# Performance work log

Hardware: AMD Instinct MI355X
Metric: run time of the kernel (lower is better)

## Reference

```python
import jax, jax.numpy as jnp
import numpy as np

C = 192          # filter_channels (= in_channels in this module)
K = 3            # kernel_size
NB = 10          # num_bins of rational-quadratic spline (VITS default)
TB = 5.0         # tail_bound
NF = 4           # number of ConvFlow steps per branch
L = 3            # DDSConv n_layers
LOG2PI = float(np.log(2.0 * np.pi))


def conv1x1(x, w, b):
    # x: (B, Cin, T), w: (Cout, Cin)
    return jnp.einsum('oi,bit->bot', w, x) + b[None, :, None]


def depthwise(x, w, b, dil):
    # x: (B, C, T), w: (C, 1, K), dilated depthwise conv, 'same' padding
    pad = dil * (K - 1) // 2
    y = jax.lax.conv_general_dilated(
        x, w, window_strides=(1,), padding=[(pad, pad)], rhs_dilation=(dil,),
        dimension_numbers=('NCH', 'OIH', 'NCH'), feature_group_count=x.shape[1])
    return y + b[None, :, None]


def layer_norm_c(x, g, b, eps=1e-5):
    # VITS LayerNorm: normalize over the channel axis (axis=1)
    m = jnp.mean(x, axis=1, keepdims=True)
    v = jnp.mean((x - m) ** 2, axis=1, keepdims=True)
    return (x - m) * jax.lax.rsqrt(v + eps) * g[None, :, None] + b[None, :, None]


def dds(x, x_mask, g, dep_w, dep_b, pw_w, pw_b, ln_g, ln_b):
    # DDSConv: dilated depth-separable conv stack with residual
    if g is not None:
        x = x + g
    for i in range(L):
        dil = K ** i
        y = depthwise(x * x_mask, dep_w[i], dep_b[i], dil)
        y = jax.nn.gelu(layer_norm_c(y, ln_g[i, 0], ln_b[i, 0]))
        y = conv1x1(y, pw_w[i], pw_b[i])
        y = jax.nn.gelu(layer_norm_c(y, ln_g[i, 1], ln_b[i, 1]))
        x = x + y  # dropout disabled in deterministic reference
    return x * x_mask


def ew_affine(z, x_mask, m, logs):
    y = (m[None, :, None] + jnp.exp(logs)[None, :, None] * z) * x_mask
    ld = jnp.sum(logs[None, :, None] * x_mask, axis=(1, 2))
    return y, ld


def rqs_forward(x_in, uw, uh, ud):
    # unconstrained rational-quadratic spline, forward direction, linear tails
    mb = 1e-3  # min bin width / height / derivative
    const = float(np.log(np.expm1(1.0 - mb)))
    inside = (x_in >= -TB) & (x_in <= TB)
    ud = jnp.pad(ud, ((0, 0), (0, 0), (0, 0), (1, 1)), constant_values=const)
    wd = jax.nn.softmax(uw, -1); wd = mb + (1.0 - mb * NB) * wd
    cw = jnp.cumsum(wd, -1)
    cw = jnp.concatenate([jnp.zeros_like(cw[..., :1]), cw], -1)
    cw = 2.0 * TB * cw - TB
    cw = cw.at[..., 0].set(-TB).at[..., -1].set(TB)
    wd = cw[..., 1:] - cw[..., :-1]
    ht = jax.nn.softmax(uh, -1); ht = mb + (1.0 - mb * NB) * ht
    ch = jnp.cumsum(ht, -1)
    ch = jnp.concatenate([jnp.zeros_like(ch[..., :1]), ch], -1)
    ch = 2.0 * TB * ch - TB
    ch = ch.at[..., 0].set(-TB).at[..., -1].set(TB)
    ht = ch[..., 1:] - ch[..., :-1]
    dv = mb + jax.nn.softplus(ud)  # (..., NB+1)
    xc = jnp.clip(x_in, -TB, TB)
    idx = jnp.clip(jnp.sum((xc[..., None] >= cw[..., :-1]).astype(jnp.int32), -1) - 1, 0, NB - 1)
    g = lambda a, i: jnp.take_along_axis(a, i[..., None], -1)[..., 0]
    icw, iw, ich, ih = g(cw, idx), g(wd, idx), g(ch, idx), g(ht, idx)
    idelta = ih / iw
    d0, d1 = g(dv, idx), g(dv, idx + 1)
    th = (xc - icw) / iw
    t1m = th * (1.0 - th)
    den = idelta + (d0 + d1 - 2.0 * idelta) * t1m
    out = ich + ih * (idelta * th * th + d0 * t1m) / den
    dnum = idelta * idelta * (d1 * th * th + 2.0 * idelta * t1m + d0 * (1.0 - th) ** 2)
    lad = jnp.log(dnum) - 2.0 * jnp.log(den)
    return jnp.where(inside, out, x_in), jnp.where(inside, lad, 0.0)


def conv_flow(z, x_mask, g, pre_w, pre_b, dep_w, dep_b, pw_w, pw_b, ln_g, ln_b, proj_w, proj_b):
    x0, x1 = z[:, :1], z[:, 1:]  # (B,1,T) each
    h = conv1x1(x0, pre_w, pre_b)
    h = dds(h, x_mask, g, dep_w, dep_b, pw_w, pw_b, ln_g, ln_b)
    h = conv1x1(h, proj_w, proj_b) * x_mask      # (B, 3*NB-1, T)
    B, _, T = h.shape
    h = h.reshape(B, 1, 3 * NB - 1, T).transpose(0, 1, 3, 2)  # (B,1,T,3*NB-1)
    s = 1.0 / np.sqrt(C)
    x1n, lad = rqs_forward(x1, h[..., :NB] * s, h[..., NB:2 * NB] * s, h[..., 2 * NB:])
    zo = jnp.concatenate([x0, x1n], 1) * x_mask
    return zo, jnp.sum(lad * x_mask, axis=(1, 2))


def _forward(x, x_mask, w, e_q, pre_w, pre_b, proj_w, proj_b,
             dds_dep_w, dds_dep_b, dds_pw_w, dds_pw_b, dds_ln_g, dds_ln_b,
             post_pre_w, post_pre_b, post_proj_w, post_proj_b,
             pdds_dep_w, pdds_dep_b, pdds_pw_w, pdds_pw_b, pdds_ln_g, pdds_ln_b,
             aff_m, aff_logs,
             f_pre_w, f_pre_b, f_dep_w, f_dep_b, f_pw_w, f_pw_b, f_ln_g, f_ln_b, f_proj_w, f_proj_b,
             paff_m, paff_logs,
             p_pre_w, p_pre_b, p_dep_w, p_dep_b, p_pw_w, p_pw_b, p_ln_g, p_ln_b, p_proj_w, p_proj_b):
    x = jax.lax.stop_gradient(x)
    h = conv1x1(x, pre_w, pre_b)
    h = dds(h, x_mask, None, dds_dep_w, dds_dep_b, dds_pw_w, dds_pw_b, dds_ln_g, dds_ln_b)
    h = conv1x1(h, proj_w, proj_b) * x_mask
    hw = conv1x1(w, post_pre_w, post_pre_b)
    hw = dds(hw, x_mask, None, pdds_dep_w, pdds_dep_b, pdds_pw_w, pdds_pw_b, pdds_ln_g, pdds_ln_b)
    hw = conv1x1(hw, post_proj_w, post_proj_b) * x_mask
    e = e_q * x_mask
    zq, ldq = ew_affine(e, x_mask, paff_m, paff_logs)
    gp = h + hw
    for i in range(NF):
        zq, ld = conv_flow(zq, x_mask, gp, p_pre_w[i], p_pre_b[i], p_dep_w[i], p_dep_b[i],
                           p_pw_w[i], p_pw_b[i], p_ln_g[i], p_ln_b[i], p_proj_w[i], p_proj_b[i])
        ldq = ldq + ld
        zq = zq[:, ::-1]  # Flip (logdet 0)
    zu, z1 = zq[:, :1], zq[:, 1:]
    u = jax.nn.sigmoid(zu) * x_mask
    z0 = (w - u) * x_mask
    ldq = ldq + jnp.sum((jax.nn.log_sigmoid(zu) + jax.nn.log_sigmoid(-zu)) * x_mask, axis=(1, 2))
    logq = jnp.sum(-0.5 * (LOG2PI + e * e) * x_mask, axis=(1, 2)) - ldq
    y0 = jnp.log(jnp.maximum(z0, 1e-5)) * x_mask  # Log flow
    ldt = jnp.sum(-y0, axis=(1, 2))
    z = jnp.concatenate([y0, z1], 1)
    z, ld = ew_affine(z, x_mask, aff_m, aff_logs)
    ldt = ldt + ld
    for i in range(NF):
        z, ld = conv_flow(z, x_mask, h, f_pre_w[i], f_pre_b[i], f_dep_w[i], f_dep_b[i],
                          f_pw_w[i], f_pw_b[i], f_ln_g[i], f_ln_b[i], f_proj_w[i], f_proj_b[i])
        ldt = ldt + ld
        z = z[:, ::-1]
    nll = jnp.sum(0.5 * (LOG2PI + z * z) * x_mask, axis=(1, 2)) - ldt
    return nll + logq  # (B,)


def setup_inputs() -> dict:
    key = jax.random.key(0)
    ks = jax.random.split(key, 24)
    B, T = 32, 768
    P = 3 * NB - 1
    r = lambda k, shape, s=0.05: jax.random.normal(k, shape, jnp.float32) * s
    d = {}
    d['x'] = jax.random.normal(ks[0], (B, C, T), jnp.float32)
    d['x_mask'] = jnp.ones((B, 1, T), jnp.float32)
    d['w'] = jax.random.uniform(ks[1], (B, 1, T), jnp.float32) * 10.0 + 1.0  # positive durations
    d['e_q'] = jax.random.normal(ks[2], (B, 2, T), jnp.float32)
    d['pre_w'] = r(ks[3], (C, C)); d['pre_b'] = jnp.zeros((C,), jnp.float32)
    d['proj_w'] = r(ks[4], (C, C)); d['proj_b'] = jnp.zeros((C,), jnp.float32)
    d['dds_dep_w'] = r(ks[5], (L, C, 1, K)); d['dds_dep_b'] = jnp.zeros((L, C), jnp.float32)
    d['dds_pw_w'] = r(ks[6], (L, C, C)); d['dds_pw_b'] = jnp.zeros((L, C), jnp.float32)
    d['dds_ln_g'] = jnp.ones((L, 2, C), jnp.float32); d['dds_ln_b'] = jnp.zeros((L, 2, C), jnp.float32)
    d['post_pre_w'] = r(ks[7], (C, 1)); d['post_pre_b'] = jnp.zeros((C,), jnp.float32)
    d['post_proj_w'] = r(ks[8], (C, C)); d['post_proj_b'] = jnp.zeros((C,), jnp.float32)
    d['pdds_dep_w'] = r(ks[9], (L, C, 1, K)); d['pdds_dep_b'] = jnp.zeros((L, C), jnp.float32)
    d['pdds_pw_w'] = r(ks[10], (L, C, C)); d['pdds_pw_b'] = jnp.zeros((L, C), jnp.float32)
    d['pdds_ln_g'] = jnp.ones((L, 2, C), jnp.float32); d['pdds_ln_b'] = jnp.zeros((L, 2, C), jnp.float32)
    d['aff_m'] = r(ks[11], (2,)); d['aff_logs'] = r(ks[12], (2,))
    d['f_pre_w'] = r(ks[13], (NF, C, 1)); d['f_pre_b'] = jnp.zeros((NF, C), jnp.float32)
    d['f_dep_w'] = r(ks[14], (NF, L, C, 1, K)); d['f_dep_b'] = jnp.zeros((NF, L, C), jnp.float32)
    d['f_pw_w'] = r(ks[15], (NF, L, C, C)); d['f_pw_b'] = jnp.zeros((NF, L, C), jnp.float32)
    d['f_ln_g'] = jnp.ones((NF, L, 2, C), jnp.float32); d['f_ln_b'] = jnp.zeros((NF, L, 2, C), jnp.float32)
    d['f_proj_w'] = r(ks[16], (NF, P, C), 0.01); d['f_proj_b'] = jnp.zeros((NF, P), jnp.float32)
    d['paff_m'] = r(ks[17], (2,)); d['paff_logs'] = r(ks[18], (2,))
    d['p_pre_w'] = r(ks[19], (NF, C, 1)); d['p_pre_b'] = jnp.zeros((NF, C), jnp.float32)
    d['p_dep_w'] = r(ks[20], (NF, L, C, 1, K)); d['p_dep_b'] = jnp.zeros((NF, L, C), jnp.float32)
    d['p_pw_w'] = r(ks[21], (NF, L, C, C)); d['p_pw_b'] = jnp.zeros((NF, L, C), jnp.float32)
    d['p_ln_g'] = jnp.ones((NF, L, 2, C), jnp.float32); d['p_ln_b'] = jnp.zeros((NF, L, 2, C), jnp.float32)
    d['p_proj_w'] = r(ks[22], (NF, P, C), 0.01); d['p_proj_b'] = jnp.zeros((NF, P), jnp.float32)
    return d


def reference(x, x_mask, w, e_q, pre_w, pre_b, proj_w, proj_b,
              dds_dep_w, dds_dep_b, dds_pw_w, dds_pw_b, dds_ln_g, dds_ln_b,
              post_pre_w, post_pre_b, post_proj_w, post_proj_b,
              pdds_dep_w, pdds_dep_b, pdds_pw_w, pdds_pw_b, pdds_ln_g, pdds_ln_b,
              aff_m, aff_logs,
              f_pre_w, f_pre_b, f_dep_w, f_dep_b, f_pw_w, f_pw_b, f_ln_g, f_ln_b, f_proj_w, f_proj_b,
              paff_m, paff_logs,
              p_pre_w, p_pre_b, p_dep_w, p_dep_b, p_pw_w, p_pw_b, p_ln_g, p_ln_b, p_proj_w, p_proj_b):
    return _forward(x, x_mask, w, e_q, pre_w, pre_b, proj_w, proj_b,
                    dds_dep_w, dds_dep_b, dds_pw_w, dds_pw_b, dds_ln_g, dds_ln_b,
                    post_pre_w, post_pre_b, post_proj_w, post_proj_b,
                    pdds_dep_w, pdds_dep_b, pdds_pw_w, pdds_pw_b, pdds_ln_g, pdds_ln_b,
                    aff_m, aff_logs,
                    f_pre_w, f_pre_b, f_dep_w, f_dep_b, f_pw_w, f_pw_b, f_ln_g, f_ln_b, f_proj_w, f_proj_b,
                    paff_m, paff_logs,
                    p_pre_w, p_pre_b, p_dep_w, p_dep_b, p_pw_w, p_pw_b, p_ln_g, p_ln_b, p_proj_w, p_proj_b)
```

## Files before the change

kernel.cpp:

```cpp
#include <hip/hip_runtime.h>
#include <math.h>

#define CC 192
#define TTT 768
#define PP 29
#define LOG2PI_F 1.8378770664093453f
#define WSLOT 36864
#define PSW 6144
#define XS 200
#define XSP 200
#define PARL 1728

typedef __attribute__((ext_vector_type(8))) short short8;
typedef __attribute__((ext_vector_type(4))) float floatx4;
typedef __attribute__((ext_vector_type(2))) float float2v;
union Frag { int4 i; short8 s; };

__device__ __forceinline__ float2v fma2(float2v a, float2v b, float2v c){
  return __builtin_elementwise_fma(a, b, c);
}
__device__ __forceinline__ float geluf(float x){
  float u = 1.5957691216057308f * (x + 0.044715f*x*x*x);
  return x * __builtin_amdgcn_rcpf(1.f + __expf(-u));
}
__device__ __forceinline__ float softplus_f(float x){
  return (x > 20.f) ? x : log1pf(__expf(x));
}
__device__ __forceinline__ float logsig_f(float x){
  return -softplus_f(-x);
}
__device__ __forceinline__ unsigned short f2bf(float f){
  unsigned int u = __builtin_bit_cast(unsigned int, f);
  u += 0x7fffu + ((u >> 16) & 1u);
  return (unsigned short)(u >> 16);
}
__device__ __forceinline__ unsigned int packbf2(float a0, float a1){
  return (unsigned int)f2bf(a0) | ((unsigned int)f2bf(a1) << 16);
}
__device__ __forceinline__ void unbf2(unsigned int u, float& lo, float& hi){
  lo = __builtin_bit_cast(float, u << 16);
  hi = __builtin_bit_cast(float, u & 0xffff0000u);
}
__device__ __forceinline__ float2v unbf2v(unsigned int u){
  float2v r;
  r.x = __builtin_bit_cast(float, u << 16);
  r.y = __builtin_bit_cast(float, u & 0xffff0000u);
  return r;
}
__device__ __forceinline__ void unp8(int4 v, float* o){
  unsigned int* p = (unsigned int*)&v;
  unbf2(p[0], o[0], o[1]); unbf2(p[1], o[2], o[3]);
  unbf2(p[2], o[4], o[5]); unbf2(p[3], o[6], o[7]);
}
__device__ __forceinline__ void f4arr(float4 v, float* o){ o[0]=v.x;o[1]=v.y;o[2]=v.z;o[3]=v.w; }
__device__ __forceinline__ float2v pick2(float4 a, float4 b, int p){
  switch(p){
    case 0: return (float2v){a.x, a.y};
    case 1: return (float2v){a.z, a.w};
    case 2: return (float2v){b.x, b.y};
    default: return (float2v){b.z, b.w};
  }
}

__global__ __launch_bounds__(256) void convert_w_k(
    const float* __restrict__ p0, const float* __restrict__ p1,
    const float* __restrict__ p2, const float* __restrict__ p3,
    const float* __restrict__ p4, const float* __restrict__ p5,
    const float* __restrict__ p6, const float* __restrict__ p7,
    const float* __restrict__ p8, unsigned short* __restrict__ Wb){
  int i = blockIdx.x*256 + threadIdx.x;
  const int totalA = 33*WSLOT;
  const int total = totalA + 8*PSW;
  if (i >= total) return;
  if (i < totalA){
    int slot = i / WSLOT, j = i % WSLOT;
    int e = j & 7, lane = (j>>3) & 63, kt = j >> 9;
    int k = kt % 6, tile = kt / 6;
    int co = tile*16 + (lane & 15);
    int kk = k*32 + (lane>>4)*8 + e;
    int r = co*CC + kk;
    const float* src;
    if      (slot == 0) src = p0 + r;
    else if (slot == 1) src = p1 + r;
    else if (slot == 2) src = p2 + r;
    else if (slot < 6)  src = p3 + (size_t)(slot-3)*WSLOT + r;
    else if (slot < 9)  src = p4 + (size_t)(slot-6)*WSLOT + r;
    else if (slot < 21) src = p5 + (size_t)(slot-9)*WSLOT + r;
    else                src = p6 + (size_t)(slot-21)*WSLOT + r;
    Wb[i] = f2bf(*src);
  } else {
    int r2 = i - totalA;
    int ps = r2 / PSW, j = r2 % PSW;
    int e = j & 7, lane = (j>>3) & 63, kt = j >> 9;
    int k = kt % 6, tile = kt / 6;
    int co = tile*16 + (lane & 15); if (co > PP-1) co = PP-1;
    int kk = k*32 + (lane>>4)*8 + e;
    const float* base = (ps < 4) ? (p7 + (size_t)ps*PP*CC) : (p8 + (size_t)(ps-4)*PP*CC);
    Wb[i] = f2bf(base[co*CC + kk]);
  }
}

__global__ __launch_bounds__(256) void pack_par_k(
    const float* __restrict__ dds_dep_w, const float* __restrict__ dds_dep_b,
    const float* __restrict__ dds_ln_g,  const float* __restrict__ dds_ln_b,
    const float* __restrict__ dds_pw_b,
    const float* __restrict__ pdds_dep_w, const float* __restrict__ pdds_dep_b,
    const float* __restrict__ pdds_ln_g,  const float* __restrict__ pdds_ln_b,
    const float* __restrict__ pdds_pw_b,
    const float* __restrict__ p_dep_w, const float* __restrict__ p_dep_b,
    const float* __restrict__ p_ln_g,  const float* __restrict__ p_ln_b,
    const float* __restrict__ p_pw_b,
    const float* __restrict__ f_dep_w, const float* __restrict__ f_dep_b,
    const float* __restrict__ f_ln_g,  const float* __restrict__ f_ln_b,
    const float* __restrict__ f_pw_b,
    float* __restrict__ P){
  int i = blockIdx.x*256 + threadIdx.x;
  const int total = 30*PARL;
  if (i >= total) return;
  int ls = i / PARL, r = i % PARL;
  int arr = r / 192, c = r % 192;
  const float *dep_w, *dep_b, *ln_g, *ln_b, *pw_b;
  int l;
  if (ls < 3){
    l = ls; dep_w = dds_dep_w; dep_b = dds_dep_b; ln_g = dds_ln_g; ln_b = dds_ln_b; pw_b = dds_pw_b;
  } else if (ls < 6){
    l = ls-3; dep_w = pdds_dep_w; dep_b = pdds_dep_b; ln_g = pdds_ln_g; ln_b = pdds_ln_b; pw_b = pdds_pw_b;
  } else if (ls < 18){
    int f = (ls-6)/3; l = (ls-6)%3;
    dep_w = p_dep_w + (size_t)f*3*CC*3; dep_b = p_dep_b + (size_t)f*3*CC;
    ln_g = p_ln_g + (size_t)f*3*2*CC;  ln_b = p_ln_b + (size_t)f*3*2*CC;
    pw_b = p_pw_b + (size_t)f*3*CC;
  } else {
    int f = (ls-18)/3; l = (ls-18)%3;
    dep_w = f_dep_w + (size_t)f*3*CC*3; dep_b = f_dep_b + (size_t)f*3*CC;
    ln_g = f_ln_g + (size_t)f*3*2*CC;  ln_b = f_ln_b + (size_t)f*3*2*CC;
    pw_b = f_pw_b + (size_t)f*3*CC;
  }
  float v;
  if      (arr < 3)  v = dep_w[((size_t)l*CC + c)*3 + arr];
  else if (arr == 3) v = dep_b[(size_t)l*CC + c];
  else if (arr == 4) v = ln_g[((size_t)l*2+0)*CC + c];
  else if (arr == 5) v = ln_b[((size_t)l*2+0)*CC + c];
  else if (arr == 6) v = ln_g[((size_t)l*2+1)*CC + c];
  else if (arr == 7) v = ln_b[((size_t)l*2+1)*CC + c];
  else               v = pw_b[(size_t)l*CC + c];
  P[i] = v;
}

__global__ __launch_bounds__(256) void transpose_x_k(
    const float* __restrict__ x, unsigned short* __restrict__ xT){
  __shared__ unsigned short tile[32*XS];
  int b = blockIdx.y, t0 = blockIdx.x*32, tid = threadIdx.x;
  int tl4 = (tid & 7)*4, cr = tid >> 3;
  #pragma unroll
  for (int rnd=0; rnd<6; rnd++){
    int c = rnd*32 + cr;
    float4 v4 = *(const float4*)(x + ((size_t)b*CC + c)*TTT + t0 + tl4);
    tile[(tl4+0)*XS + c] = f2bf(v4.x);
    tile[(tl4+1)*XS + c] = f2bf(v4.y);
    tile[(tl4+2)*XS + c] = f2bf(v4.z);
    tile[(tl4+3)*XS + c] = f2bf(v4.w);
  }
  __syncthreads();
  #pragma unroll
  for (int k=0;k<3;k++){
    int task = k*256 + tid;
    int row = task/24, cn = task%24;
    *(int4*)(xT + ((size_t)b*TTT + t0 + row)*CC + cn*8) = *(const int4*)&tile[row*XS + cn*8];
  }
}

__global__ __launch_bounds__(256) void conv_cc_k(
    const unsigned short* __restrict__ in, const unsigned short* __restrict__ Wsw,
    const float* __restrict__ bias, const float* __restrict__ mask,
    const unsigned short* __restrict__ addsrc, unsigned short* __restrict__ outb, int mode){
  __shared__ unsigned short bufX[32*XS];
  __shared__ unsigned short bufY[32*XS];
  __shared__ float marr[32];
  int b = blockIdx.y, t0 = blockIdx.x*32, tid = threadIdx.x;
  #pragma unroll
  for (int k=0;k<3;k++){
    int task = k*256 + tid;
    int row = task/24, cn = task%24;
    const unsigned short* src = in + ((size_t)b*TTT + t0 + row)*CC + cn*8;
    *(int4*)&bufX[row*XS + cn*8] = *(const int4*)src;
    if (mode == 2){
      const unsigned short* s2 = addsrc + ((size_t)b*TTT + t0 + row)*CC + cn*8;
      *(int4*)&bufY[row*XS + cn*8] = *(const int4*)s2;
    }
  }
  if (tid >= 128 && tid < 160) marr[tid-128] = mask[(size_t)b*TTT + t0 + (tid-128)];
  __syncthreads();
  int w = tid >> 6, lane = tid & 63;
  int n16 = lane & 15, quad = lane >> 4;
  Frag af[3][6];
  #pragma unroll
  for (int ct=0; ct<3; ct++){
    int tile = w*3 + ct;
    #pragma unroll
    for (int k=0;k<6;k++)
      af[ct][k].i = *(const int4*)(Wsw + ((size_t)(tile*6 + k)*64 + lane)*8);
  }
  floatx4 acc[3][2];
  #pragma unroll
  for (int ct=0;ct<3;ct++)
    #pragma unroll
    for (int tt=0;tt<2;tt++)
      acc[ct][tt] = (floatx4){0.f,0.f,0.f,0.f};
  #pragma unroll
  for (int k=0;k<6;k++){
    Frag bf[2];
    #pragma unroll
    for (int tt=0;tt<2;tt++)
      bf[tt].i = *(const int4*)&bufX[(tt*16+n16)*XS + k*32 + quad*8];
    #pragma unroll
    for (int ct=0;ct<3;ct++)
      #pragma unroll
      for (int tt=0;tt<2;tt++)
        acc[ct][tt] = __builtin_amdgcn_mfma_f32_16x16x32_bf16(af[ct][k].s, bf[tt].s, acc[ct][tt], 0,0,0);
  }
  __syncthreads();
  #pragma unroll
  for (int ct=0;ct<3;ct++){
    int cobase = w*48 + ct*16 + quad*4;
    float4 b4 = *(const float4*)(bias + cobase);
    float ba[4] = {b4.x, b4.y, b4.z, b4.w};
    #pragma unroll
    for (int tt=0;tt<2;tt++){
      int t = tt*16 + n16;
      float mv = (mode >= 1) ? marr[t] : 1.f;
      float av[4] = {0.f,0.f,0.f,0.f};
      if (mode == 2){
        uint2 uy = *(uint2*)&bufY[t*XS + cobase];
        unbf2(uy.x, av[0], av[1]); unbf2(uy.y, av[2], av[3]);
      }
      float hh[4];
      #pragma unroll
      for (int r=0;r<4;r++){
        float v = acc[ct][tt][r] + ba[r];
        if (mode >= 1) v *= mv;
        if (mode == 2) v += av[r];
        hh[r] = v;
      }
      uint2 wv; wv.x = packbf2(hh[0], hh[1]); wv.y = packbf2(hh[2], hh[3]);
      *(uint2*)&bufX[t*XS + cobase] = wv;
    }
  }
  __syncthreads();
  #pragma unroll
  for (int k=0;k<3;k++){
    int task = k*256 + tid;
    int row = task/24, cn = task%24;
    *(int4*)(outb + ((size_t)b*TTT + t0 + row)*CC + cn*8) = *(const int4*)&bufX[row*XS + cn*8];
  }
}

template<int DIL, int SPLITF>
__device__ __forceinline__ void dds_layer(
    unsigned short* __restrict__ ping,
    const float* __restrict__ pl,
    float* __restrict__ pnd, const float* __restrict__ pns,
    const float* __restrict__ mrow,
    float (* __restrict__ sqx)[2][2],
    const unsigned short* __restrict__ WL,
    int tid, int w, int lane, int n16, int quad, int row){
  constexpr int NT = SPLITF ? 6 : 12;
  const int tb = SPLITF ? ((w & 1)*6) : 0;
  const int rowL = SPLITF ? (16 + (w>>1)*16 + n16) : row;
  Frag bfr[6];
  floatx4 acc[NT];
  {
    int iL = rowL - DIL; iL = iL < 0 ? 0 : iL;
    int iR = rowL + DIL; iR = iR > 63 ? 63 : iR;
    float2v vv[24];
    float2v s2v = {0.f,0.f}, q2v = {0.f,0.f};
    #pragma unroll
    for (int j=0;j<6;j++){
      int kk = j*32 + quad*8;
      int4 L4 = *(const int4*)&ping[iL*XSP + kk];
      int4 C4 = *(const int4*)&ping[rowL*XSP + kk];
      int4 R4 = *(const int4*)&ping[iR*XSP + kk];
      unsigned int* Lp = (unsigned int*)&L4;
      unsigned int* Cp = (unsigned int*)&C4;
      unsigned int* Rp = (unsigned int*)&R4;
      float4 w0a = *(const float4*)&pl[kk],       w0b = *(const float4*)&pl[kk+4];
      float4 w1a = *(const float4*)&pl[192+kk],   w1b = *(const float4*)&pl[192+kk+4];
      float4 w2a = *(const float4*)&pl[384+kk],   w2b = *(const float4*)&pl[384+kk+4];
      float4 dba = *(const float4*)&pl[576+kk],   dbb = *(const float4*)&pl[576+kk+4];
      #pragma unroll
      for (int p=0;p<4;p++){
        float2v val = fma2(pick2(w0a,w0b,p), unbf2v(Lp[p]),
                      fma2(pick2(w1a,w1b,p), unbf2v(Cp[p]),
                      fma2(pick2(w2a,w2b,p), unbf2v(Rp[p]), pick2(dba,dbb,p))));
        vv[j*4+p] = val;
        s2v += val;
        q2v = fma2(val, val, q2v);
      }
    }
    float s = s2v.x + s2v.y, q = q2v.x + q2v.y;
    s += __shfl_xor(s, 16); s += __shfl_xor(s, 32);
    q += __shfl_xor(q, 16); q += __shfl_xor(q, 32);
    float mm = s*(1.f/CC);
    float rr = rsqrtf(q*(1.f/CC) - mm*mm + 1e-5f);
    float2v mm2 = {mm,mm}, rr2 = {rr,rr};
    #pragma unroll
    for (int j=0;j<6;j++){
      int kk = j*32 + quad*8;
      float4 g0a = *(const float4*)&pl[768+kk], g0b = *(const float4*)&pl[768+kk+4];
      float4 b0a = *(const float4*)&pl[960+kk], b0b = *(const float4*)&pl[960+kk+4];
      unsigned int wwp[4];
      #pragma unroll
      for (int p=0;p<4;p++){
        float2v a = fma2((vv[j*4+p]-mm2)*rr2, pick2(g0a,g0b,p), pick2(b0a,b0b,p));
        wwp[p] = packbf2(geluf(a.x), geluf(a.y));
      }
      bfr[j].i = make_int4((int)wwp[0], (int)wwp[1], (int)wwp[2], (int)wwp[3]);
    }
  }
  __syncthreads();
  if (pns){
    #pragma unroll
    for (int k=0;k<7;k++){
      int i2 = k*256 + tid;
      if (i2 < PARL) pnd[i2] = pns[i2];
    }
  }
  {
    Frag afb[2][6];
    #pragma unroll
    for (int k=0;k<6;k++)
      afb[0][k].i = *(const int4*)(WL + ((size_t)((tb+0)*6 + k)*64 + lane)*8);
    #pragma unroll
    for (int tile=0; tile<NT; tile++){
      int cur = tile & 1, nxt = cur ^ 1;
      if (tile < NT-1){
        #pragma unroll
        for (int k=0;k<6;k++)
          afb[nxt][k].i = *(const int4*)(WL + ((size_t)((tb+tile+1)*6 + k)*64 + lane)*8);
      }
      acc[tile] = (floatx4){0.f,0.f,0.f,0.f};
      #pragma unroll
      for (int k=0;k<6;k++)
        acc[tile] = __builtin_amdgcn_mfma_f32_16x16x32_bf16(afb[cur][k].s, bfr[k].s, acc[tile], 0,0,0);
    }
  }
  float2v s2p = {0.f,0.f}, q2p = {0.f,0.f};
  #pragma unroll
  for (int tile=0; tile<NT; tile++){
    int co = (tb+tile)*16 + quad*4;
    float4 pbv = *(const float4*)&pl[1536+co];
    acc[tile][0] += pbv.x; acc[tile][1] += pbv.y;
    acc[tile][2] += pbv.z; acc[tile][3] += pbv.w;
    float2v v01 = {acc[tile][0], acc[tile][1]};
    float2v v23 = {acc[tile][2], acc[tile][3]};
    s2p += v01 + v23;
    q2p = fma2(v01, v01, q2p);
    q2p = fma2(v23, v23, q2p);
  }
  float s2 = s2p.x + s2p.y, q2 = q2p.x + q2p.y;
  s2 += __shfl_xor(s2, 16); s2 += __shfl_xor(s2, 32);
  q2 += __shfl_xor(q2, 16); q2 += __shfl_xor(q2, 32);
  if constexpr (SPLITF){
    int r16 = rowL - 16;
    if (quad == 0){ sqx[r16][w&1][0] = s2; sqx[r16][w&1][1] = q2; }
    __syncthreads();
    int oh = (w&1)^1;
    s2 += sqx[r16][oh][0];
    q2 += sqx[r16][oh][1];
  }
  float cmP = s2*(1.f/CC);
  float crP = rsqrtf(q2*(1.f/CC) - cmP*cmP + 1e-5f);
  float mc = mrow[rowL];
  float2v mc2 = {mc,mc};
  float2v cm2 = {cmP,cmP}, cr2 = {crP,crP};
  #pragma unroll
  for (int tile=0; tile<NT; tile++){
    int co = (tb+tile)*16 + quad*4;
    float4 g1v = *(const float4*)&pl[1152+co];
    float4 b1v = *(const float4*)&pl[1344+co];
    uint2 ux = *(uint2*)&ping[rowL*XSP + co];
    float2v x01 = unbf2v(ux.x), x23 = unbf2v(ux.y);
    float2v v01 = {acc[tile][0], acc[tile][1]};
    float2v v23 = {acc[tile][2], acc[tile][3]};
    float2v a01 = fma2((v01-cm2)*cr2, (float2v){g1v.x,g1v.y}, (float2v){b1v.x,b1v.y});
    float2v a23 = fma2((v23-cm2)*cr2, (float2v){g1v.z,g1v.w}, (float2v){b1v.z,b1v.w});
    float2v h01 = (x01 + (float2v){geluf(a01.x), geluf(a01.y)}) * mc2;
    float2v h23 = (x23 + (float2v){geluf(a23.x), geluf(a23.y)}) * mc2;
    uint2 wv;
    wv.x = packbf2(h01.x, h01.y);
    wv.y = packbf2(h23.x, h23.y);
    *(uint2*)&ping[rowL*XSP + co] = wv;
  }
  __syncthreads();
}

__global__ __launch_bounds__(256,3) void mega_dds_k(
    const unsigned short* __restrict__ in,
    const float* __restrict__ zsrc, int zstride,
    const unsigned short* __restrict__ g,
    unsigned short* __restrict__ outb,
    const float* __restrict__ mask,
    const float* __restrict__ parP,
    const float* __restrict__ pw1, const float* __restrict__ pb1,
    const unsigned short* __restrict__ Wsw,
    int srcmode, int outmode,
    const unsigned short* __restrict__ projW, const float* __restrict__ projB,
    float* __restrict__ z, int zs, float* __restrict__ acco){
  __shared__ unsigned short ping[64*XSP];
  __shared__ float par[2][PARL];
  __shared__ float mrow[64];
  __shared__ float sqx[32][2][2];
  float* pro = par[0];

  int b = blockIdx.y, t0 = blockIdx.x*32, tid = threadIdx.x;
  int ws0 = t0 - 16;
  int w = tid >> 6, lane = tid & 63;
  int n16 = lane & 15, quad = lane >> 4;
  int row = w*16 + n16;
  const float* mkb = mask + (size_t)b*TTT;

  if (tid < 64){
    int gt = ws0 + tid;
    bool inr = (gt >= 0) && (gt < TTT);
    int gc = gt < 0 ? 0 : (gt > TTT-1 ? TTT-1 : gt);
    mrow[tid] = inr ? mkb[gc] : 0.f;
  }
  #pragma unroll
  for (int k=0;k<7;k++){
    int i2 = k*256 + tid;
    if (i2 < PARL) par[0][i2] = parP[i2];
  }
  if (srcmode == 0){
    #pragma unroll
    for (int k=0;k<6;k++){
      int task = k*256 + tid;
      int r = task/24, cn = task%24, c0 = cn*8;
      int gt = ws0 + r;
      bool inr = (gt >= 0) && (gt < TTT);
      int gc = gt < 0 ? 0 : (gt > TTT-1 ? TTT-1 : gt);
      float mv = inr ? mkb[gc] : 0.f;
      float hv[8];
      unp8(*(const int4*)(in + ((size_t)b*TTT + gc)*CC + c0), hv);
      int4 pk;
      pk.x = (int)packbf2(hv[0]*mv, hv[1]*mv); pk.y = (int)packbf2(hv[2]*mv, hv[3]*mv);
      pk.z = (int)packbf2(hv[4]*mv, hv[5]*mv); pk.w = (int)packbf2(hv[6]*mv, hv[7]*mv);
      *(int4*)&ping[r*XSP + c0] = pk;
    }
  } else {
    #pragma unroll
    for (int k=0;k<6;k++){
      int task = k*256 + tid;
      int r = task/24, cn = task%24, c0 = cn*8;
      int gt = ws0 + r;
      bool inr = (gt >= 0) && (gt < TTT);
      int gc = gt < 0 ? 0 : (gt > TTT-1 ? TTT-1 : gt);
      float mv = inr ? mkb[gc] : 0.f;
      float zv = inr ? zsrc[(size_t)b*zstride + gc] : 0.f;
      float hv[8];
      if (g){
        unp8(*(const int4*)(g + ((size_t)b*TTT + gc)*CC + c0), hv);
      } else {
        #pragma unroll
        for (int e=0;e<8;e++) hv[e] = 0.f;
      }
      float4 pwa = *(const float4*)(pw1 + c0);
      float4 pwb2 = *(const float4*)(pw1 + c0 + 4);
      float4 pba = *(const float4*)(pb1 + c0);
      float4 pbb2 = *(const float4*)(pb1 + c0 + 4);
      float pwv[8], pbv[8];
      f4arr(pwa, pwv); f4arr(pwb2, pwv+4);
      f4arr(pba, pbv); f4arr(pbb2, pbv+4);
      float ov[8];
      #pragma unroll
      for (int e=0;e<8;e++) ov[e] = (hv[e] + fmaf(pwv[e], zv, pbv[e]))*mv;
      int4 pk;
      pk.x = (int)packbf2(ov[0], ov[1]); pk.y = (int)packbf2(ov[2], ov[3]);
      pk.z = (int)packbf2(ov[4], ov[5]); pk.w = (int)packbf2(ov[6], ov[7]);
      *(int4*)&ping[r*XSP + c0] = pk;
    }
  }
  __syncthreads();

  dds_layer<1,0>(ping, par[0], par[1], parP + (size_t)1*PARL, mrow, sqx,
                 Wsw + 0*(size_t)WSLOT, tid, w, lane, n16, quad, row);
  dds_layer<3,0>(ping, par[1], par[0], parP + (size_t)2*PARL, mrow, sqx,
                 Wsw + 1*(size_t)WSLOT, tid, w, lane, n16, quad, row);
  dds_layer<9,1>(ping, par[0], nullptr, nullptr, mrow, sqx,
                 Wsw + 2*(size_t)WSLOT, tid, w, lane, n16, quad, row);

  if (outmode == 0){
    #pragma unroll
    for (int k=0;k<3;k++){
      int task = k*256 + tid;
      int r = task/24, cn = task%24, c0 = cn*8;
      *(int4*)(outb + ((size_t)b*TTT + t0 + r)*CC + c0) = *(const int4*)&ping[(16+r)*XSP + c0];
    }
    return;
  }

  {
    int ctp = w & 1;
    int prow = 16 + (w>>1)*16 + n16;
    Frag afp[6];
    #pragma unroll
    for (int k=0;k<6;k++)
      afp[k].i = *(const int4*)(projW + ((size_t)(ctp*6 + k)*64 + lane)*8);
    Frag bfp[6];
    #pragma unroll
    for (int k=0;k<6;k++)
      bfp[k].i = *(const int4*)&ping[prow*XSP + k*32 + quad*8];
    floatx4 acc2 = (floatx4){0.f,0.f,0.f,0.f};
    #pragma unroll
    for (int k=0;k<6;k++)
      acc2 = __builtin_amdgcn_mfma_f32_16x16x32_bf16(afp[k].s, bfp[k].s, acc2, 0,0,0);
    int rt = prow - 16;
    float mv = mrow[prow];
    #pragma unroll
    for (int r=0;r<4;r++){
      int co = ctp*16 + quad*4 + r;
      if (co < PP) pro[rt*30 + co] = (acc2[r] + projB[co]) * mv;
    }
  }
  __syncthreads();
  if (tid < 32){
    const float scv = 0.07216878364870323f;
    int tg = t0 + tid;
    float m = mrow[16+tid];
    float* z0p = z + ((size_t)b*2 + zs)*TTT + tg;
    float* z1p = z + ((size_t)b*2 + (1-zs))*TTT + tg;
    float xs = *z1p;
    float uw[10], uh[10], ud[9];
    #pragma unroll
    for (int k=0;k<10;k++) uw[k]=pro[tid*30+k]*scv;
    #pragma unroll
    for (int k=0;k<10;k++) uh[k]=pro[tid*30+10+k]*scv;
    #pragma unroll
    for (int k=0;k<9;k++)  ud[k]=pro[tid*30+20+k];
    bool inside = (xs >= -5.f) && (xs <= 5.f);
    float xc = fminf(fmaxf(xs,-5.f),5.f);
    float mx=uw[0];
    #pragma unroll
    for (int k=1;k<10;k++) mx=fmaxf(mx,uw[k]);
    float sw=0.f; float wd[10];
    #pragma unroll
    for (int k=0;k<10;k++){ wd[k]=__expf(uw[k]-mx); sw+=wd[k]; }
    float invw = 1.f/sw;
    #pragma unroll
    for (int k=0;k<10;k++) wd[k]=fmaf(0.99f*invw, wd[k], 1e-3f);
    float mh=uh[0];
    #pragma unroll
    for (int k=1;k<10;k++) mh=fmaxf(mh,uh[k]);
    float sh=0.f; float ht[10];
    #pragma unroll
    for (int k=0;k<10;k++){ ht[k]=__expf(uh[k]-mh); sh+=ht[k]; }
    float invh = 1.f/sh;
    #pragma unroll
    for (int k=0;k<10;k++) ht[k]=fmaf(0.99f*invh, ht[k], 1e-3f);
    float cw=-5.f, icw=-5.f, iw=1.f; int idx=0;
    #pragma unroll
    for (int i2=0;i2<10;i2++){
      float nw = (i2==9) ? 5.f : fmaf(10.f, wd[i2], cw);
      if (cw <= xc){ idx=i2; icw=cw; iw=nw-cw; }
      cw=nw;
    }
    float ch=-5.f, ich=-5.f, ih=1.f;
    #pragma unroll
    for (int i2=0;i2<10;i2++){
      float nh = (i2==9) ? 5.f : fmaf(10.f, ht[i2], ch);
      if (i2==idx){ ich=ch; ih=nh-ch; }
      ch=nh;
    }
    const float UDC = logf(expm1f(0.999f));
    float d0=1.f, d1=1.f;
    #pragma unroll
    for (int k=0;k<11;k++){
      float uu = (k==0 || k==10) ? UDC : ud[k-1];
      float dk = 1e-3f + softplus_f(uu);
      if (k==idx)   d0=dk;
      if (k==idx+1) d1=dk;
    }
    float idel = ih/iw;
    float th = (xc-icw)/iw;
    float t1m = th*(1.f-th);
    float den = idel + (d0+d1-2.f*idel)*t1m;
    float outv = ich + ih*(idel*th*th + d0*t1m)/den;
    float omt = 1.f-th;
    float dnum = idel*idel*(d1*th*th + 2.f*idel*t1m + d0*omt*omt);
    float lad = logf(dnum) - 2.f*logf(den);
    float y = inside ? outv : xs;
    lad = inside ? lad : 0.f;
    *z1p = y*m;
    *z0p = (*z0p)*m;
    float lm = lad*m;
    lm += __shfl_xor(lm, 1); lm += __shfl_xor(lm, 2);
    lm += __shfl_xor(lm, 4); lm += __shfl_xor(lm, 8);
    lm += __shfl_xor(lm, 16);
    if (tid == 0) atomicAdd(acco + b, -lm);
  }
}

__global__ __launch_bounds__(256) void init_z_k(
    const float* __restrict__ e_q, const float* __restrict__ mask,
    const float* __restrict__ pm, const float* __restrict__ pl,
    float* __restrict__ z, float* __restrict__ acc){
  __shared__ float red[256];
  int b = blockIdx.y; int t = blockIdx.x*256 + threadIdx.x;
  float m = mask[(size_t)b*TTT + t];
  float pl0=pl[0], pl1=pl[1];
  float e0 = e_q[((size_t)b*2+0)*TTT + t]*m;
  float e1 = e_q[((size_t)b*2+1)*TTT + t]*m;
  z[((size_t)b*2+0)*TTT + t] = fmaf(__expf(pl0), e0, pm[0])*m;
  z[((size_t)b*2+1)*TTT + t] = fmaf(__expf(pl1), e1, pm[1])*m;
  float contrib = -0.5f*(LOG2PI_F + e0*e0)*m - 0.5f*(LOG2PI_F + e1*e1)*m - (pl0+pl1)*m;
  int tid = threadIdx.x;
  red[tid] = contrib;
  __syncthreads();
  for (int o=128;o>0;o>>=1){ if (tid<o) red[tid]+=red[tid+o]; __syncthreads(); }
  if (tid==0) atomicAdd(acc+b, red[0]);
}

__global__ __launch_bounds__(256) void final_pre_k(
    float* __restrict__ z, const float* __restrict__ w_in, const float* __restrict__ mask,
    const float* __restrict__ am, const float* __restrict__ al, float* __restrict__ acc){
  __shared__ float red[256];
  int b = blockIdx.y; int t = blockIdx.x*256 + threadIdx.x;
  float m = mask[(size_t)b*TTT + t];
  float zu  = z[((size_t)b*2+0)*TTT + t];
  float z1v = z[((size_t)b*2+1)*TTT + t];
  float wv  = w_in[(size_t)b*TTT + t];
  float u  = m / (1.f + __expf(-zu));
  float z0 = (wv - u)*m;
  float y0 = logf(fmaxf(z0, 1e-5f))*m;
  float al0=al[0], al1=al[1];
  z[((size_t)b*2+0)*TTT + t] = fmaf(__expf(al0), y0,  am[0])*m;
  z[((size_t)b*2+1)*TTT + t] = fmaf(__expf(al1), z1v, am[1])*m;
  float contrib = -(logsig_f(zu)+logsig_f(-zu))*m + y0 - (al0+al1)*m;
  int tid = threadIdx.x;
  red[tid] = contrib;
  __syncthreads();
  for (int o=128;o>0;o>>=1){ if (tid<o) red[tid]+=red[tid+o]; __syncthreads(); }
  if (tid==0) atomicAdd(acc+b, red[0]);
}

__global__ __launch_bounds__(256) void final_post_k(
    const float* __restrict__ z, const float* __restrict__ mask, float* __restrict__ acc){
  __shared__ float red[256];
  int b = blockIdx.y; int t = blockIdx.x*256 + threadIdx.x;
  float m = mask[(size_t)b*TTT + t];
  float z0 = z[((size_t)b*2+0)*TTT + t];
  float z1 = z[((size_t)b*2+1)*TTT + t];
  float contrib = 0.5f*(LOG2PI_F + z0*z0)*m + 0.5f*(LOG2PI_F + z1*z1)*m;
  int tid = threadIdx.x;
  red[tid] = contrib;
  __syncthreads();
  for (int o=128;o>0;o>>=1){ if (tid<o) red[tid]+=red[tid+o]; __syncthreads(); }
  if (tid==0) atomicAdd(acc+b, red[0]);
}

__global__ void write_out_k(const float* __restrict__ acc, float* __restrict__ out, int n){
  int i = threadIdx.x;
  if (i < n) out[i] = acc[i];
}

extern "C" void kernel_launch(void* const* d_in, const int* in_sizes, int n_in,
                              void* d_out, int out_size, void* d_ws, size_t ws_size,
                              hipStream_t stream){
  (void)n_in; (void)out_size; (void)ws_size;
  const float* x         = (const float*)d_in[0];
  const float* mask      = (const float*)d_in[1];
  const float* w_in      = (const float*)d_in[2];
  const float* e_q       = (const float*)d_in[3];
  const float* pre_w     = (const float*)d_in[4];
  const float* pre_b     = (const float*)d_in[5];
  const float* proj_w    = (const float*)d_in[6];
  const float* proj_b    = (const float*)d_in[7];
  const float* dds_dep_w = (const float*)d_in[8];
  const float* dds_dep_b = (const float*)d_in[9];
  const float* dds_pw_w  = (const float*)d_in[10];
  const float* dds_pw_b  = (const float*)d_in[11];
  const float* dds_ln_g  = (const float*)d_in[12];
  const float* dds_ln_b  = (const float*)d_in[13];
  const float* post_pre_w  = (const float*)d_in[14];
  const float* post_pre_b  = (const float*)d_in[15];
  const float* post_proj_w = (const float*)d_in[16];
  const float* post_proj_b = (const float*)d_in[17];
  const float* pdds_dep_w  = (const float*)d_in[18];
  const float* pdds_dep_b  = (const float*)d_in[19];
  const float* pdds_pw_w   = (const float*)d_in[20];
  const float* pdds_pw_b   = (const float*)d_in[21];
  const float* pdds_ln_g   = (const float*)d_in[22];
  const float* pdds_ln_b   = (const float*)d_in[23];
  const float* aff_m    = (const float*)d_in[24];
  const float* aff_logs = (const float*)d_in[25];
  const float* f_pre_w  = (const float*)d_in[26];
  const float* f_pre_b  = (const float*)d_in[27];
  const float* f_dep_w  = (const float*)d_in[28];
  const float* f_dep_b  = (const float*)d_in[29];
  const float* f_pw_w   = (const float*)d_in[30];
  const float* f_pw_b   = (const float*)d_in[31];
  const float* f_ln_g   = (const float*)d_in[32];
  const float* f_ln_b   = (const float*)d_in[33];
  const float* f_proj_w = (const float*)d_in[34];
  const float* f_proj_b = (const float*)d_in[35];
  const float* paff_m    = (const float*)d_in[36];
  const float* paff_logs = (const float*)d_in[37];
  const float* p_pre_w  = (const float*)d_in[38];
  const float* p_pre_b  = (const float*)d_in[39];
  const float* p_dep_w  = (const float*)d_in[40];
  const float* p_dep_b  = (const float*)d_in[41];
  const float* p_pw_w   = (const float*)d_in[42];
  const float* p_pw_b   = (const float*)d_in[43];
  const float* p_ln_g   = (const float*)d_in[44];
  const float* p_ln_b   = (const float*)d_in[45];
  const float* p_proj_w = (const float*)d_in[46];
  const float* p_proj_b = (const float*)d_in[47];

  int Bn = in_sizes[0] / (CC*TTT);
  size_t big2 = (size_t)Bn*CC*TTT;
  unsigned short* xT = (unsigned short*)d_ws;
  unsigned short* A  = xT + big2;
  unsigned short* Bb = A  + big2;
  unsigned short* H  = Bb + big2;
  unsigned short* GP = H  + big2;
  unsigned short* Wb = GP + big2;
  size_t wtot = 33*(size_t)WSLOT + 8*(size_t)PSW;
  float* parP = (float*)(Wb + ((wtot + 7) & ~(size_t)7));
  float* zbuf = parP + 30*(size_t)PARL;
  float* acc  = zbuf + (size_t)Bn*2*TTT;

  hipMemsetAsync(acc, 0, Bn*sizeof(float), stream);
  convert_w_k<<<(int)((wtot + 255)/256), 256, 0, stream>>>(
      pre_w, proj_w, post_proj_w, dds_pw_w, pdds_pw_w, p_pw_w, f_pw_w,
      p_proj_w, f_proj_w, Wb);
  pack_par_k<<<(30*PARL + 255)/256, 256, 0, stream>>>(
      dds_dep_w, dds_dep_b, dds_ln_g, dds_ln_b, dds_pw_b,
      pdds_dep_w, pdds_dep_b, pdds_ln_g, pdds_ln_b, pdds_pw_b,
      p_dep_w, p_dep_b, p_ln_g, p_ln_b, p_pw_b,
      f_dep_w, f_dep_b, f_ln_g, f_ln_b, f_pw_b, parP);

  dim3 g32(TTT/32, Bn), g256(TTT/256, Bn);
  dim3 b256(256);

  unsigned short* W_pre      = Wb + 0*(size_t)WSLOT;
  unsigned short* W_proj     = Wb + 1*(size_t)WSLOT;
  unsigned short* W_postproj = Wb + 2*(size_t)WSLOT;
  unsigned short* W_dds      = Wb + 3*(size_t)WSLOT;
  unsigned short* W_pdds     = Wb + 6*(size_t)WSLOT;
  unsigned short* W_ppw      = Wb + 9*(size_t)WSLOT;
  unsigned short* W_fpw      = Wb + 21*(size_t)WSLOT;
  unsigned short* W_pproj    = Wb + 33*(size_t)WSLOT;
  unsigned short* W_fproj    = W_pproj + 4*(size_t)PSW;

  transpose_x_k<<<g32, b256, 0, stream>>>(x, xT);

  conv_cc_k<<<g32, b256, 0, stream>>>(xT, W_pre, pre_b, mask, nullptr, A, 0);
  mega_dds_k<<<g32, b256, 0, stream>>>(A, nullptr, 0, nullptr, Bb, mask,
      parP + 0*(size_t)3*PARL, nullptr, nullptr,
      W_dds, 0, 0, nullptr, nullptr, nullptr, 0, acc);
  conv_cc_k<<<g32, b256, 0, stream>>>(Bb, W_proj, proj_b, mask, nullptr, H, 1);

  mega_dds_k<<<g32, b256, 0, stream>>>(nullptr, w_in, TTT, nullptr, A, mask,
      parP + 1*(size_t)3*PARL, post_pre_w, post_pre_b,
      W_pdds, 1, 0, nullptr, nullptr, nullptr, 0, acc);
  conv_cc_k<<<g32, b256, 0, stream>>>(A, W_postproj, post_proj_b, mask, H, GP, 2);

  init_z_k<<<g256, b256, 0, stream>>>(e_q, mask, paff_m, paff_logs, zbuf, acc);

  for (int f=0; f<4; f++){
    int s = f & 1;
    mega_dds_k<<<g32, b256, 0, stream>>>(nullptr, zbuf + (size_t)s*TTT, 2*TTT, GP, nullptr, mask,
        parP + (size_t)(2+f)*3*PARL,
        p_pre_w + (size_t)f*CC, p_pre_b + (size_t)f*CC,
        W_ppw + (size_t)f*3*WSLOT, 1, 1,
        W_pproj + (size_t)f*PSW, p_proj_b + (size_t)f*PP, zbuf, s, acc);
  }

  final_pre_k<<<g256, b256, 0, stream>>>(zbuf, w_in, mask, aff_m, aff_logs, acc);

  for (int f=0; f<4; f++){
    int s = f & 1;
    mega_dds_k<<<g32, b256, 0, stream>>>(nullptr, zbuf + (size_t)s*TTT, 2*TTT, H, nullptr, mask,
        parP + (size_t)(6+f)*3*PARL,
        f_pre_w + (size_t)f*CC, f_pre_b + (size_t)f*CC,
        W_fpw + (size_t)f*3*WSLOT, 1, 1,
        W_fproj + (size_t)f*PSW, f_proj_b + (size_t)f*PP, zbuf, s, acc);
  }

  final_post_k<<<g256, b256, 0, stream>>>(zbuf, mask, acc);
  write_out_k<<<1, 64, 0, stream>>>(acc, (float*)d_out, Bn);
}
```

Baseline: 781.2 us.

## Fuse transpose into pre-conv and 1x1 projection convs into DDS kernel epilogue

The separate transpose kernel is merged into the first 1x1 conv, so x goes from fp32 global memory straight into shared memory as bf16 and is consumed there. The proj and post_proj 1x1 convs, with their mask and residual add, now run as an epilogue of mega_dds_k (outmode 2) on the tile already in shared memory. This removes three kernel launches and the global write and read of the intermediate buffers xT, Bb and A. In exchange mega_dds_k gets more parameters and a larger code path, which may raise register pressure under its occupancy bound of 3.

```diff
diff --git a/kernel.cpp b/kernel.cpp
--- a/kernel.cpp
+++ b/kernel.cpp
@@ -147,49 +147,21 @@
   P[i] = v;
 }
 
-__global__ __launch_bounds__(256) void transpose_x_k(
-    const float* __restrict__ x, unsigned short* __restrict__ xT){
-  __shared__ unsigned short tile[32*XS];
+__global__ __launch_bounds__(256) void trans_conv_k(
+    const float* __restrict__ x, const unsigned short* __restrict__ Wsw,
+    const float* __restrict__ bias, unsigned short* __restrict__ outb){
+  __shared__ unsigned short bufX[32*XS];
   int b = blockIdx.y, t0 = blockIdx.x*32, tid = threadIdx.x;
   int tl4 = (tid & 7)*4, cr = tid >> 3;
   #pragma unroll
   for (int rnd=0; rnd<6; rnd++){
     int c = rnd*32 + cr;
     float4 v4 = *(const float4*)(x + ((size_t)b*CC + c)*TTT + t0 + tl4);
-    tile[(tl4+0)*XS + c] = f2bf(v4.x);
-    tile[(tl4+1)*XS + c] = f2bf(v4.y);
-    tile[(tl4+2)*XS + c] = f2bf(v4.z);
-    tile[(tl4+3)*XS + c] = f2bf(v4.w);
-  }
-  __syncthreads();
-  #pragma unroll
-  for (int k=0;k<3;k++){
-    int task = k*256 + tid;
-    int row = task/24, cn = task%24;
-    *(int4*)(xT + ((size_t)b*TTT + t0 + row)*CC + cn*8) = *(const int4*)&tile[row*XS + cn*8];
-  }
-}
-
-__global__ __launch_bounds__(256) void conv_cc_k(
-    const unsigned short* __restrict__ in, const unsigned short* __restrict__ Wsw,
-    const float* __restrict__ bias, const float* __restrict__ mask,
-    const unsigned short* __restrict__ addsrc, unsigned short* __restrict__ outb, int mode){
-  __shared__ unsigned short bufX[32*XS];
-  __shared__ unsigned short bufY[32*XS];
-  __shared__ float marr[32];
-  int b = blockIdx.y, t0 = blockIdx.x*32, tid = threadIdx.x;
-  #pragma unroll
-  for (int k=0;k<3;k++){
-    int task = k*256 + tid;
-    int row = task/24, cn = task%24;
-    const unsigned short* src = in + ((size_t)b*TTT + t0 + row)*CC + cn*8;
-    *(int4*)&bufX[row*XS + cn*8] = *(const int4*)src;
-    if (mode == 2){
-      const unsigned short* s2 = addsrc + ((size_t)b*TTT + t0 + row)*CC + cn*8;
-      *(int4*)&bufY[row*XS + cn*8] = *(const int4*)s2;
-    }
-  }
-  if (tid >= 128 && tid < 160) marr[tid-128] = mask[(size_t)b*TTT + t0 + (tid-128)];
+    bufX[(tl4+0)*XS + c] = f2bf(v4.x);
+    bufX[(tl4+1)*XS + c] = f2bf(v4.y);
+    bufX[(tl4+2)*XS + c] = f2bf(v4.z);
+    bufX[(tl4+3)*XS + c] = f2bf(v4.w);
+  }
   __syncthreads();
   int w = tid >> 6, lane = tid & 63;
   int n16 = lane & 15, quad = lane >> 4;
@@ -224,25 +196,12 @@
   for (int ct=0;ct<3;ct++){
     int cobase = w*48 + ct*16 + quad*4;
     float4 b4 = *(const float4*)(bias + cobase);
-    float ba[4] = {b4.x, b4.y, b4.z, b4.w};
     #pragma unroll
     for (int tt=0;tt<2;tt++){
       int t = tt*16 + n16;
-      float mv = (mode >= 1) ? marr[t] : 1.f;
-      float av[4] = {0.f,0.f,0.f,0.f};
-      if (mode == 2){
-        uint2 uy = *(uint2*)&bufY[t*XS + cobase];
-        unbf2(uy.x, av[0], av[1]); unbf2(uy.y, av[2], av[3]);
-      }
-      float hh[4];
-      #pragma unroll
-      for (int r=0;r<4;r++){
-        float v = acc[ct][tt][r] + ba[r];
-        if (mode >= 1) v *= mv;
-        if (mode == 2) v += av[r];
-        hh[r] = v;
-      }
-      uint2 wv; wv.x = packbf2(hh[0], hh[1]); wv.y = packbf2(hh[2], hh[3]);
+      uint2 wv;
+      wv.x = packbf2(acc[ct][tt][0] + b4.x, acc[ct][tt][1] + b4.y);
+      wv.y = packbf2(acc[ct][tt][2] + b4.z, acc[ct][tt][3] + b4.w);
       *(uint2*)&bufX[t*XS + cobase] = wv;
     }
   }
@@ -398,14 +357,16 @@
     const unsigned short* __restrict__ in,
     const float* __restrict__ zsrc, int zstride,
     const unsigned short* __restrict__ g,
-    unsigned short* __restrict__ outb,
     const float* __restrict__ mask,
     const float* __restrict__ parP,
     const float* __restrict__ pw1, const float* __restrict__ pb1,
     const unsigned short* __restrict__ Wsw,
     int srcmode, int outmode,
     const unsigned short* __restrict__ projW, const float* __restrict__ projB,
-    float* __restrict__ z, int zs, float* __restrict__ acco){
+    float* __restrict__ z, int zs, float* __restrict__ acco,
+    const unsigned short* __restrict__ cvW, const float* __restrict__ cvB,
+    const unsigned short* __restrict__ addsrc, unsigned short* __restrict__ cvout,
+    int cvmode){
   __shared__ unsigned short ping[64*XSP];
   __shared__ float par[2][PARL];
   __shared__ float mrow[64];
@@ -488,12 +449,76 @@
   dds_layer<9,1>(ping, par[0], nullptr, nullptr, mrow, sqx,
                  Wsw + 2*(size_t)WSLOT, tid, w, lane, n16, quad, row);
 
-  if (outmode == 0){
+  if (outmode == 2){
+    if (cvmode == 2){
+      #pragma unroll
+      for (int k=0;k<3;k++){
+        int task = k*256 + tid;
+        int r = task/24, cn = task%24;
+        int dr = r + ((r >= 16) ? 32 : 0);
+        *(int4*)&ping[dr*XSP + cn*8] =
+            *(const int4*)(addsrc + ((size_t)b*TTT + t0 + r)*CC + cn*8);
+      }
+    }
+    Frag af[3][6];
+    #pragma unroll
+    for (int ct=0; ct<3; ct++){
+      int tile = w*3 + ct;
+      #pragma unroll
+      for (int k=0;k<6;k++)
+        af[ct][k].i = *(const int4*)(cvW + ((size_t)(tile*6 + k)*64 + lane)*8);
+    }
+    floatx4 acc2[3][2];
+    #pragma unroll
+    for (int ct=0;ct<3;ct++)
+      #pragma unroll
+      for (int tt=0;tt<2;tt++)
+        acc2[ct][tt] = (floatx4){0.f,0.f,0.f,0.f};
+    #pragma unroll
+    for (int k=0;k<6;k++){
+      Frag bf[2];
+      #pragma unroll
+      for (int tt=0;tt<2;tt++)
+        bf[tt].i = *(const int4*)&ping[(16 + tt*16 + n16)*XSP + k*32 + quad*8];
+      #pragma unroll
+      for (int ct=0;ct<3;ct++)
+        #pragma unroll
+        for (int tt=0;tt<2;tt++)
+          acc2[ct][tt] = __builtin_amdgcn_mfma_f32_16x16x32_bf16(af[ct][k].s, bf[tt].s, acc2[ct][tt], 0,0,0);
+    }
+    __syncthreads();
+    #pragma unroll
+    for (int ct=0;ct<3;ct++){
+      int cobase = w*48 + ct*16 + quad*4;
+      float4 b4 = *(const float4*)(cvB + cobase);
+      float ba[4] = {b4.x, b4.y, b4.z, b4.w};
+      #pragma unroll
+      for (int tt=0;tt<2;tt++){
+        int t = tt*16 + n16;
+        float mv = mrow[16 + t];
+        float av[4] = {0.f,0.f,0.f,0.f};
+        if (cvmode == 2){
+          int hr = t + ((t >= 16) ? 32 : 0);
+          uint2 uy = *(uint2*)&ping[hr*XSP + cobase];
+          unbf2(uy.x, av[0], av[1]); unbf2(uy.y, av[2], av[3]);
+        }
+        float hh[4];
+        #pragma unroll
+        for (int r=0;r<4;r++){
+          float v = (acc2[ct][tt][r] + ba[r]) * mv;
+          if (cvmode == 2) v += av[r];
+          hh[r] = v;
+        }
+        uint2 wv; wv.x = packbf2(hh[0], hh[1]); wv.y = packbf2(hh[2], hh[3]);
+        *(uint2*)&ping[(16 + t)*XSP + cobase] = wv;
+      }
+    }
+    __syncthreads();
     #pragma unroll
     for (int k=0;k<3;k++){
       int task = k*256 + tid;
       int r = task/24, cn = task%24, c0 = cn*8;
-      *(int4*)(outb + ((size_t)b*TTT + t0 + r)*CC + c0) = *(const int4*)&ping[(16+r)*XSP + c0];
+      *(int4*)(cvout + ((size_t)b*TTT + t0 + r)*CC + c0) = *(const int4*)&ping[(16+r)*XSP + c0];
     }
     return;
   }
@@ -751,39 +776,39 @@
   unsigned short* W_pproj    = Wb + 33*(size_t)WSLOT;
   unsigned short* W_fproj    = W_pproj + 4*(size_t)PSW;
 
-  transpose_x_k<<<g32, b256, 0, stream>>>(x, xT);
-
-  conv_cc_k<<<g32, b256, 0, stream>>>(xT, W_pre, pre_b, mask, nullptr, A, 0);
-  mega_dds_k<<<g32, b256, 0, stream>>>(A, nullptr, 0, nullptr, Bb, mask,
+  trans_conv_k<<<g32, b256, 0, stream>>>(x, W_pre, pre_b, A);
+  mega_dds_k<<<g32, b256, 0, stream>>>(A, nullptr, 0, nullptr, mask,
       parP + 0*(size_t)3*PARL, nullptr, nullptr,
-      W_dds, 0, 0, nullptr, nullptr, nullptr, 0, acc);
-  conv_cc_k<<<g32, b256, 0, stream>>>(Bb, W_proj, proj_b, mask, nullptr, H, 1);
-
-  mega_dds_k<<<g32, b256, 0, stream>>>(nullptr, w_in, TTT, nullptr, A, mask,
+      W_dds, 0, 2, nullptr, nullptr, nullptr, 0, acc,
+      W_proj, proj_b, nullptr, H, 1);
+
+  mega_dds_k<<<g32, b256, 0, stream>>>(nullptr, w_in, TTT, nullptr, mask,
       parP + 1*(size_t)3*PARL, post_pre_w, post_pre_b,
-      W_pdds, 1, 0, nullptr, nullptr, nullptr, 0, acc);
-  conv_cc_k<<<g32, b256, 0, stream>>>(A, W_postproj, post_proj_b, mask, H, GP, 2);
+      W_pdds, 1, 2, nullptr, nullptr, nullptr, 0, acc,
+      W_postproj, post_proj_b, H, GP, 2);
 
   init_z_k<<<g256, b256, 0, stream>>>(e_q, mask, paff_m, paff_logs, zbuf, acc);
 
   for (int f=0; f<4; f++){
     int s = f & 1;
-    mega_dds_k<<<g32, b256, 0, stream>>>(nullptr, zbuf + (size_t)s*TTT, 2*TTT, GP, nullptr, mask,
+    mega_dds_k<<<g32, b256, 0, stream>>>(nullptr, zbuf + (size_t)s*TTT, 2*TTT, GP, mask,
         parP + (size_t)(2+f)*3*PARL,
         p_pre_w + (size_t)f*CC, p_pre_b + (size_t)f*CC,
         W_ppw + (size_t)f*3*WSLOT, 1, 1,
-        W_pproj + (size_t)f*PSW, p_proj_b + (size_t)f*PP, zbuf, s, acc);
+        W_pproj + (size_t)f*PSW, p_proj_b + (size_t)f*PP, zbuf, s, acc,
+        nullptr, nullptr, nullptr, nullptr, 0);
   }
 
   final_pre_k<<<g256, b256, 0, stream>>>(zbuf, w_in, mask, aff_m, aff_logs, acc);
 
   for (int f=0; f<4; f++){
     int s = f & 1;
-    mega_dds_k<<<g32, b256, 0, stream>>>(nullptr, zbuf + (size_t)s*TTT, 2*TTT, H, nullptr, mask,
+    mega_dds_k<<<g32, b256, 0, stream>>>(nullptr, zbuf + (size_t)s*TTT, 2*TTT, H, mask,
         parP + (size_t)(6+f)*3*PARL,
         f_pre_w + (size_t)f*CC, f_pre_b + (size_t)f*CC,
         W_fpw + (size_t)f*3*WSLOT, 1, 1,
-        W_fproj + (size_t)f*PSW, f_proj_b + (size_t)f*PP, zbuf, s, acc);
+        W_fproj + (size_t)f*PSW, f_proj_b + (size_t)f*PP, zbuf, s, acc,
+        nullptr, nullptr, nullptr, nullptr, 0);
   }
 
   final_post_k<<<g256, b256, 0, stream>>>(zbuf, mask, acc);
```

Result: faster. 741.9 us (-5.0%).
